# Kernel tuning notes

Hardware: AMD Instinct MI355X
Metric: run time of the kernel (lower is better)

Reference implementation:

```python
import jax, jax.numpy as jnp
import numpy as np


def setup_inputs() -> dict:
    key = jax.random.key(0)
    ks = jax.random.split(key, 8)
    B, T, U = 4, 256, 64
    A, D, H, V = 512, 640, 640, 1024
    inp = {
        "encoder_output": jax.random.normal(ks[0], (B, T, A), dtype=jnp.float32),
        "decoder_output": jax.random.normal(ks[1], (B, U, D), dtype=jnp.float32),
        "W_enc": jax.random.normal(ks[2], (A, H), dtype=jnp.float32) / np.sqrt(A),
        "b_enc": jnp.zeros((H,), dtype=jnp.float32),
        "W_dec": jax.random.normal(ks[3], (D, H), dtype=jnp.float32) / np.sqrt(D),
        "b_dec": jnp.zeros((H,), dtype=jnp.float32),
        "W_out": jax.random.normal(ks[4], (H, V), dtype=jnp.float32) / np.sqrt(H),
        "b_out": jnp.zeros((V,), dtype=jnp.float32),
    }
    return inp


def reference(encoder_output, decoder_output, W_enc, b_enc, W_dec, b_dec, W_out, b_out):
    # project encoder (B,T,A)->(B,T,H) and decoder (B,U,D)->(B,U,H)
    enc = encoder_output @ W_enc + b_enc
    dec = decoder_output @ W_dec + b_dec
    # broadcast-add to (B,T,U,H), tanh, project to vocab, log-softmax
    z = jnp.tanh(enc[:, :, None, :] + dec[:, None, :, :])
    logits = z @ W_out + b_out  # (B,T,U,V)
    return jax.nn.log_softmax(logits, axis=-1)
```

## Files before the change

### kernel.cpp

```cpp
#include <hip/hip_runtime.h>
#include <hip/hip_bf16.h>
#include <cstdint>

#define BB 4
#define TT 256
#define UB 64
#define AA 512
#define DD 640
#define HH 640
#define VV 1024

typedef __attribute__((ext_vector_type(8))) short short8;
typedef __attribute__((ext_vector_type(4))) float f32x4;

__device__ __forceinline__ unsigned short f2bf(float f) {
    unsigned u = __builtin_bit_cast(unsigned, f);
    u += 0x7fffu + ((u >> 16) & 1u);
    return (unsigned short)(u >> 16);
}

__device__ __forceinline__ float fast_tanh(float x) {
    return 1.0f - 2.0f / (1.0f + __expf(2.0f * x));
}

__global__ __launch_bounds__(256) void kpack(const float* __restrict__ W,
                                             unsigned short* __restrict__ wp) {
    __shared__ float tile[32][64];
    const int kb  = blockIdx.x >> 4;
    const int nbg = blockIdx.x & 15;
    const int tid = threadIdx.x;
#pragma unroll
    for (int i = 0; i < 8; ++i) {
        int idx = tid + (i << 8);
        int r = idx >> 6, c = idx & 63;
        tile[r][c] = W[(size_t)(kb * 32 + r) * VV + nbg * 64 + c];
    }
    __syncthreads();
    const int hi  = tid & 3;
    const int np  = (tid >> 2) & 15;
    const int nbl = tid >> 6;
    __align__(16) unsigned short v[8];
#pragma unroll
    for (int j = 0; j < 8; ++j)
        v[j] = f2bf(tile[hi * 8 + j][nbl * 16 + np]);
    size_t off = (size_t)((kb * 64 + nbg * 4 + nbl) * 512 + np * 32 + hi * 8);
    *reinterpret_cast<uint4*>(wp + off) = *reinterpret_cast<const uint4*>(v);
}

__global__ __launch_bounds__(640) void kproj(
    const float* __restrict__ enc_in, const float* __restrict__ dec_in,
    const float* __restrict__ We, const float* __restrict__ be,
    const float* __restrict__ Wd, const float* __restrict__ bd,
    float* __restrict__ enc_out, float* __restrict__ dec_out) {
    __shared__ float rows[8][DD];
    const int bi = blockIdx.x;
    const float *in, *W, *bias;
    float* out;
    int K, row0;
    if (bi < 128) { in = enc_in; W = We; bias = be; out = enc_out; K = AA; row0 = bi * 8; }
    else          { in = dec_in; W = Wd; bias = bd; out = dec_out; K = DD; row0 = (bi - 128) * 8; }
    const int tid = threadIdx.x;
    for (int r = 0; r < 8; ++r)
        for (int k = tid; k < K; k += 640)
            rows[r][k] = in[(size_t)(row0 + r) * K + k];
    __syncthreads();
    const int col = tid;
    float acc[8] = {0.f, 0.f, 0.f, 0.f, 0.f, 0.f, 0.f, 0.f};
    for (int k = 0; k < K; ++k) {
        float w = W[(size_t)k * HH + col];
#pragma unroll
        for (int r = 0; r < 8; ++r) acc[r] = fmaf(rows[r][k], w, acc[r]);
    }
    float bbv = bias[col];
#pragma unroll
    for (int r = 0; r < 8; ++r)
        out[(size_t)(row0 + r) * HH + col] = acc[r] + bbv;
}

__global__ __launch_bounds__(512, 2) void kmain(
    const float* __restrict__ encp, const float* __restrict__ decp,
    const unsigned short* __restrict__ wp, const float* __restrict__ bo,
    float* __restrict__ out) {
    __shared__ __align__(16) unsigned char zb[UB * 1280];
    __shared__ __align__(16) float red1[UB][8];
    __shared__ __align__(16) float red2[UB][8];
    const int bt   = blockIdx.x;
    const int b    = bt >> 8;
    const int tid  = threadIdx.x;
    const int lane = tid & 63;
    const int wv   = tid >> 6;
    const int lo   = lane & 15;
    const int hi   = lane >> 4;
    const float* encr = encp + (size_t)bt * HH;
    const float* decr = decp + (size_t)b * UB * HH;

#pragma unroll
    for (int i = 0; i < 10; ++i) {
        int c  = tid + i * 512;
        int u  = c / 80;
        int h0 = (c - u * 80) * 8;
        const float4* dp = reinterpret_cast<const float4*>(decr + (size_t)u * HH + h0);
        const float4* ep = reinterpret_cast<const float4*>(encr + h0);
        float4 d0 = dp[0], d1 = dp[1];
        float4 e0 = ep[0], e1 = ep[1];
        __align__(16) unsigned short zs[8];
        zs[0] = f2bf(fast_tanh(e0.x + d0.x));
        zs[1] = f2bf(fast_tanh(e0.y + d0.y));
        zs[2] = f2bf(fast_tanh(e0.z + d0.z));
        zs[3] = f2bf(fast_tanh(e0.w + d0.w));
        zs[4] = f2bf(fast_tanh(e1.x + d1.x));
        zs[5] = f2bf(fast_tanh(e1.y + d1.y));
        zs[6] = f2bf(fast_tanh(e1.z + d1.z));
        zs[7] = f2bf(fast_tanh(e1.w + d1.w));
        unsigned addr = (unsigned)(u * 1280 + h0 * 2) ^ ((unsigned)(u & 7) << 4);
        *reinterpret_cast<uint4*>(zb + addr) = *reinterpret_cast<const uint4*>(zs);
    }
    __syncthreads();

    f32x4 acc[4][8];
#pragma unroll
    for (int mf = 0; mf < 4; ++mf)
#pragma unroll
        for (int nf = 0; nf < 8; ++nf)
            acc[mf][nf] = (f32x4){0.f, 0.f, 0.f, 0.f};
    const int nb0 = wv * 8;
#pragma unroll 2
    for (int kb = 0; kb < 20; ++kb) {
        short8 af[4];
#pragma unroll
        for (int mf = 0; mf < 4; ++mf) {
            int row = mf * 16 + lo;
            unsigned addr = (unsigned)(row * 1280 + kb * 64 + hi * 16) ^
                            ((unsigned)(row & 7) << 4);
            af[mf] = *reinterpret_cast<const short8*>(zb + addr);
        }
#pragma unroll
        for (int nf = 0; nf < 8; ++nf) {
            const unsigned short* p =
                wp + (size_t)((kb * 64 + nb0 + nf) * 512 + lo * 32 + hi * 8);
            short8 bf = *reinterpret_cast<const short8*>(p);
#pragma unroll
            for (int mf = 0; mf < 4; ++mf)
                acc[mf][nf] = __builtin_amdgcn_mfma_f32_16x16x32_bf16(
                    af[mf], bf, acc[mf][nf], 0, 0, 0);
        }
    }

    const int n0 = wv * 128;
    float bbv[8];
#pragma unroll
    for (int nf = 0; nf < 8; ++nf) bbv[nf] = bo[n0 + nf * 16 + lo];
#pragma unroll
    for (int mf = 0; mf < 4; ++mf)
#pragma unroll
        for (int nf = 0; nf < 8; ++nf) {
            acc[mf][nf][0] += bbv[nf];
            acc[mf][nf][1] += bbv[nf];
            acc[mf][nf][2] += bbv[nf];
            acc[mf][nf][3] += bbv[nf];
        }

#pragma unroll
    for (int mf = 0; mf < 4; ++mf)
#pragma unroll
        for (int rg = 0; rg < 4; ++rg) {
            float v = acc[mf][0][rg];
#pragma unroll
            for (int nf = 1; nf < 8; ++nf) v = fmaxf(v, acc[mf][nf][rg]);
            v = fmaxf(v, __shfl_xor(v, 1));
            v = fmaxf(v, __shfl_xor(v, 2));
            v = fmaxf(v, __shfl_xor(v, 4));
            v = fmaxf(v, __shfl_xor(v, 8));
            if (lo == 0) red1[mf * 16 + hi * 4 + rg][wv] = v;
        }
    __syncthreads();
    float rmax[4][4];
#pragma unroll
    for (int mf = 0; mf < 4; ++mf)
#pragma unroll
        for (int rg = 0; rg < 4; ++rg) {
            int row = mf * 16 + hi * 4 + rg;
            const float4* r4 = reinterpret_cast<const float4*>(&red1[row][0]);
            float4 x = r4[0], y = r4[1];
            rmax[mf][rg] = fmaxf(fmaxf(fmaxf(x.x, x.y), fmaxf(x.z, x.w)),
                                 fmaxf(fmaxf(y.x, y.y), fmaxf(y.z, y.w)));
        }
#pragma unroll
    for (int mf = 0; mf < 4; ++mf)
#pragma unroll
        for (int rg = 0; rg < 4; ++rg) {
            float s = 0.f;
#pragma unroll
            for (int nf = 0; nf < 8; ++nf)
                s += __expf(acc[mf][nf][rg] - rmax[mf][rg]);
            s += __shfl_xor(s, 1);
            s += __shfl_xor(s, 2);
            s += __shfl_xor(s, 4);
            s += __shfl_xor(s, 8);
            if (lo == 0) red2[mf * 16 + hi * 4 + rg][wv] = s;
        }
    __syncthreads();
    float lz[4][4];
#pragma unroll
    for (int mf = 0; mf < 4; ++mf)
#pragma unroll
        for (int rg = 0; rg < 4; ++rg) {
            int row = mf * 16 + hi * 4 + rg;
            const float4* r4 = reinterpret_cast<const float4*>(&red2[row][0]);
            float4 x = r4[0], y = r4[1];
            float s = (x.x + x.y) + (x.z + x.w) + (y.x + y.y) + (y.z + y.w);
            lz[mf][rg] = rmax[mf][rg] + __logf(s);
        }
    float* outbase = out + (size_t)bt * UB * VV;
#pragma unroll
    for (int mf = 0; mf < 4; ++mf)
#pragma unroll
        for (int rg = 0; rg < 4; ++rg) {
            int row = mf * 16 + hi * 4 + rg;
            float* orow = outbase + (size_t)row * VV + n0 + lo;
#pragma unroll
            for (int nf = 0; nf < 8; ++nf)
                orow[nf * 16] = acc[mf][nf][rg] - lz[mf][rg];
        }
}

extern "C" void kernel_launch(void* const* d_in, const int* in_sizes, int n_in,
                              void* d_out, int out_size, void* d_ws, size_t ws_size,
                              hipStream_t stream) {
    const float* enc_in = (const float*)d_in[0];
    const float* dec_in = (const float*)d_in[1];
    const float* We     = (const float*)d_in[2];
    const float* be     = (const float*)d_in[3];
    const float* Wd     = (const float*)d_in[4];
    const float* bd     = (const float*)d_in[5];
    const float* Wo     = (const float*)d_in[6];
    const float* bo     = (const float*)d_in[7];
    float* out = (float*)d_out;

    float* ws   = (float*)d_ws;
    float* encp = ws;
    float* decp = ws + 1024 * 640;
    unsigned short* wp = (unsigned short*)(ws + 1024 * 640 + 256 * 640);

    kpack<<<320, 256, 0, stream>>>(Wo, wp);
    kproj<<<160, 640, 0, stream>>>(enc_in, dec_in, We, be, Wd, bd, encp, decp);
    kmain<<<1024, 512, 0, stream>>>(encp, decp, wp, bo, out);
}
```

Measured before the change: 517.6 us.

## Tile projection GEMM in shared memory and halve kmain's z buffer

The projection kernel changes from a per-column dot product over 8 cached rows to a 64x64 shared-memory tiled SGEMM with register prefetch and 4x4 per-thread outputs, launched as 200 blocks of 256 threads. The main kernel now builds the tanh z tile in two halves of the hidden dimension, so the LDS buffer shrinks from 80KB to 40KB. The smaller LDS footprint is meant to let more blocks fit per CU and improve occupancy. The cost is an extra pair of barriers per block, and the z build for the second half can no longer overlap as freely with the first half's MFMA work.

```diff
diff --git a/kernel.cpp b/kernel.cpp
--- a/kernel.cpp
+++ b/kernel.cpp
@@ -47,41 +47,68 @@
     *reinterpret_cast<uint4*>(wp + off) = *reinterpret_cast<const uint4*>(v);
 }
 
-__global__ __launch_bounds__(640) void kproj(
+__global__ __launch_bounds__(256) void kproj(
     const float* __restrict__ enc_in, const float* __restrict__ dec_in,
     const float* __restrict__ We, const float* __restrict__ be,
     const float* __restrict__ Wd, const float* __restrict__ bd,
     float* __restrict__ enc_out, float* __restrict__ dec_out) {
-    __shared__ float rows[8][DD];
+    __shared__ float As[16][68];
+    __shared__ float Bs[16][68];
     const int bi = blockIdx.x;
-    const float *in, *W, *bias;
-    float* out;
-    int K, row0;
-    if (bi < 128) { in = enc_in; W = We; bias = be; out = enc_out; K = AA; row0 = bi * 8; }
-    else          { in = dec_in; W = Wd; bias = bd; out = dec_out; K = DD; row0 = (bi - 128) * 8; }
-    const int tid = threadIdx.x;
-    for (int r = 0; r < 8; ++r)
-        for (int k = tid; k < K; k += 640)
-            rows[r][k] = in[(size_t)(row0 + r) * K + k];
-    __syncthreads();
-    const int col = tid;
-    float acc[8] = {0.f, 0.f, 0.f, 0.f, 0.f, 0.f, 0.f, 0.f};
-    for (int k = 0; k < K; ++k) {
-        float w = W[(size_t)k * HH + col];
-#pragma unroll
-        for (int r = 0; r < 8; ++r) acc[r] = fmaf(rows[r][k], w, acc[r]);
-    }
-    float bbv = bias[col];
-#pragma unroll
-    for (int r = 0; r < 8; ++r)
-        out[(size_t)(row0 + r) * HH + col] = acc[r] + bbv;
+    const float *A, *W, *bias;
+    float* C;
+    int K, bm, bn;
+    if (bi < 160) { A = enc_in; W = We; bias = be; C = enc_out; K = AA; bm = bi / 10; bn = bi - bm * 10; }
+    else { int bj = bi - 160; A = dec_in; W = Wd; bias = bd; C = dec_out; K = DD; bm = bj / 10; bn = bj - bm * 10; }
+    const int tid  = threadIdx.x;
+    const int row0 = bm * 64, n0 = bn * 64;
+    const int tm = tid & 15, tn = tid >> 4;
+    const int am = tid & 63, akq = tid >> 6;
+    const int bk = tid >> 4, bn4 = (tid & 15) * 4;
+
+    float acc[4][4] = {};
+    float4 a4 = *reinterpret_cast<const float4*>(A + (size_t)(row0 + am) * K + akq * 4);
+    float4 b4 = *reinterpret_cast<const float4*>(W + (size_t)bk * HH + n0 + bn4);
+
+    for (int k0 = 0; k0 < K; k0 += 16) {
+        As[akq * 4 + 0][am] = a4.x;
+        As[akq * 4 + 1][am] = a4.y;
+        As[akq * 4 + 2][am] = a4.z;
+        As[akq * 4 + 3][am] = a4.w;
+        *reinterpret_cast<float4*>(&Bs[bk][bn4]) = b4;
+        __syncthreads();
+        if (k0 + 16 < K) {
+            a4 = *reinterpret_cast<const float4*>(A + (size_t)(row0 + am) * K + k0 + 16 + akq * 4);
+            b4 = *reinterpret_cast<const float4*>(W + (size_t)(k0 + 16 + bk) * HH + n0 + bn4);
+        }
+#pragma unroll
+        for (int kk = 0; kk < 16; ++kk) {
+            float4 av = *reinterpret_cast<const float4*>(&As[kk][tm * 4]);
+            float4 bv = *reinterpret_cast<const float4*>(&Bs[kk][tn * 4]);
+            float a_[4] = {av.x, av.y, av.z, av.w};
+            float b_[4] = {bv.x, bv.y, bv.z, bv.w};
+#pragma unroll
+            for (int i = 0; i < 4; ++i)
+#pragma unroll
+                for (int j = 0; j < 4; ++j)
+                    acc[i][j] = fmaf(a_[i], b_[j], acc[i][j]);
+        }
+        __syncthreads();
+    }
+    float bv0 = bias[n0 + tn * 4 + 0], bv1 = bias[n0 + tn * 4 + 1];
+    float bv2 = bias[n0 + tn * 4 + 2], bv3 = bias[n0 + tn * 4 + 3];
+#pragma unroll
+    for (int i = 0; i < 4; ++i) {
+        float4 o = {acc[i][0] + bv0, acc[i][1] + bv1, acc[i][2] + bv2, acc[i][3] + bv3};
+        *reinterpret_cast<float4*>(C + (size_t)(row0 + tm * 4 + i) * HH + n0 + tn * 4) = o;
+    }
 }
 
 __global__ __launch_bounds__(512, 2) void kmain(
     const float* __restrict__ encp, const float* __restrict__ decp,
     const unsigned short* __restrict__ wp, const float* __restrict__ bo,
     float* __restrict__ out) {
-    __shared__ __align__(16) unsigned char zb[UB * 1280];
+    __shared__ __align__(16) unsigned char zb[UB * 640];
     __shared__ __align__(16) float red1[UB][8];
     __shared__ __align__(16) float red2[UB][8];
     const int bt   = blockIdx.x;
@@ -93,29 +120,7 @@
     const int hi   = lane >> 4;
     const float* encr = encp + (size_t)bt * HH;
     const float* decr = decp + (size_t)b * UB * HH;
-
-#pragma unroll
-    for (int i = 0; i < 10; ++i) {
-        int c  = tid + i * 512;
-        int u  = c / 80;
-        int h0 = (c - u * 80) * 8;
-        const float4* dp = reinterpret_cast<const float4*>(decr + (size_t)u * HH + h0);
-        const float4* ep = reinterpret_cast<const float4*>(encr + h0);
-        float4 d0 = dp[0], d1 = dp[1];
-        float4 e0 = ep[0], e1 = ep[1];
-        __align__(16) unsigned short zs[8];
-        zs[0] = f2bf(fast_tanh(e0.x + d0.x));
-        zs[1] = f2bf(fast_tanh(e0.y + d0.y));
-        zs[2] = f2bf(fast_tanh(e0.z + d0.z));
-        zs[3] = f2bf(fast_tanh(e0.w + d0.w));
-        zs[4] = f2bf(fast_tanh(e1.x + d1.x));
-        zs[5] = f2bf(fast_tanh(e1.y + d1.y));
-        zs[6] = f2bf(fast_tanh(e1.z + d1.z));
-        zs[7] = f2bf(fast_tanh(e1.w + d1.w));
-        unsigned addr = (unsigned)(u * 1280 + h0 * 2) ^ ((unsigned)(u & 7) << 4);
-        *reinterpret_cast<uint4*>(zb + addr) = *reinterpret_cast<const uint4*>(zs);
-    }
-    __syncthreads();
+    const int nb0 = wv * 8;
 
     f32x4 acc[4][8];
 #pragma unroll
@@ -123,27 +128,55 @@
 #pragma unroll
         for (int nf = 0; nf < 8; ++nf)
             acc[mf][nf] = (f32x4){0.f, 0.f, 0.f, 0.f};
-    const int nb0 = wv * 8;
-#pragma unroll 2
-    for (int kb = 0; kb < 20; ++kb) {
-        short8 af[4];
-#pragma unroll
-        for (int mf = 0; mf < 4; ++mf) {
-            int row = mf * 16 + lo;
-            unsigned addr = (unsigned)(row * 1280 + kb * 64 + hi * 16) ^
-                            ((unsigned)(row & 7) << 4);
-            af[mf] = *reinterpret_cast<const short8*>(zb + addr);
-        }
-#pragma unroll
-        for (int nf = 0; nf < 8; ++nf) {
-            const unsigned short* p =
-                wp + (size_t)((kb * 64 + nb0 + nf) * 512 + lo * 32 + hi * 8);
-            short8 bf = *reinterpret_cast<const short8*>(p);
-#pragma unroll
-            for (int mf = 0; mf < 4; ++mf)
-                acc[mf][nf] = __builtin_amdgcn_mfma_f32_16x16x32_bf16(
-                    af[mf], bf, acc[mf][nf], 0, 0, 0);
-        }
+
+#pragma unroll
+    for (int half = 0; half < 2; ++half) {
+#pragma unroll
+        for (int i = 0; i < 5; ++i) {
+            int c  = tid + i * 512;
+            int u  = c / 40;
+            int h0 = (c - u * 40) * 8;
+            const float4* dp = reinterpret_cast<const float4*>(decr + (size_t)u * HH + half * 320 + h0);
+            const float4* ep = reinterpret_cast<const float4*>(encr + half * 320 + h0);
+            float4 d0 = dp[0], d1 = dp[1];
+            float4 e0 = ep[0], e1 = ep[1];
+            __align__(16) unsigned short zs[8];
+            zs[0] = f2bf(fast_tanh(e0.x + d0.x));
+            zs[1] = f2bf(fast_tanh(e0.y + d0.y));
+            zs[2] = f2bf(fast_tanh(e0.z + d0.z));
+            zs[3] = f2bf(fast_tanh(e0.w + d0.w));
+            zs[4] = f2bf(fast_tanh(e1.x + d1.x));
+            zs[5] = f2bf(fast_tanh(e1.y + d1.y));
+            zs[6] = f2bf(fast_tanh(e1.z + d1.z));
+            zs[7] = f2bf(fast_tanh(e1.w + d1.w));
+            unsigned addr = (unsigned)(u * 640 + h0 * 2) ^ ((unsigned)(u & 7) << 4);
+            *reinterpret_cast<uint4*>(zb + addr) = *reinterpret_cast<const uint4*>(zs);
+        }
+        __syncthreads();
+
+#pragma unroll
+        for (int kb = 0; kb < 10; ++kb) {
+            const int kbg = half * 10 + kb;
+            short8 af[4];
+#pragma unroll
+            for (int mf = 0; mf < 4; ++mf) {
+                int row = mf * 16 + lo;
+                unsigned addr = (unsigned)(row * 640 + kb * 64 + hi * 16) ^
+                                ((unsigned)(row & 7) << 4);
+                af[mf] = *reinterpret_cast<const short8*>(zb + addr);
+            }
+#pragma unroll
+            for (int nf = 0; nf < 8; ++nf) {
+                const unsigned short* p =
+                    wp + (size_t)((kbg * 64 + nb0 + nf) * 512 + lo * 32 + hi * 8);
+                short8 bf = *reinterpret_cast<const short8*>(p);
+#pragma unroll
+                for (int mf = 0; mf < 4; ++mf)
+                    acc[mf][nf] = __builtin_amdgcn_mfma_f32_16x16x32_bf16(
+                        af[mf], bf, acc[mf][nf], 0, 0, 0);
+            }
+        }
+        __syncthreads();
     }
 
     const int n0 = wv * 128;
@@ -243,6 +276,6 @@
     unsigned short* wp = (unsigned short*)(ws + 1024 * 640 + 256 * 640);
 
     kpack<<<320, 256, 0, stream>>>(Wo, wp);
-    kproj<<<160, 640, 0, stream>>>(enc_in, dec_in, We, be, Wd, bd, encp, decp);
+    kproj<<<200, 256, 0, stream>>>(enc_in, dec_in, We, be, Wd, bd, encp, decp);
     kmain<<<1024, 512, 0, stream>>>(encp, decp, wp, bo, out);
 }
```

Result: faster. 475.7 us (-8.1%).
